# Kernel tuning notes

Hardware: AMD Instinct MI355X
Metric: run time of the kernel (lower is better)

Reference implementation:

```python
import jax, jax.numpy as jnp
import numpy as np

N_ATOMS = 100000
K_NBR = 64
N_STRUCT = 32
HID = 128


def _energy(x, W1, w2, mask, batch_idx):
    # x: [N, K, 3] neighbor displacement vectors; surrogate per-edge energy MLP
    h = jnp.tanh(jnp.einsum('nkc,cd->nkd', x, W1))          # [N, K, HID]
    e = jnp.einsum('nkd,d->nk', h, w2)                       # [N, K]
    e = jnp.where(mask, 0.0, e)                              # zero padded neighbors
    per_atom = e.sum(axis=1)                                 # [N]
    return jax.ops.segment_sum(per_atom, batch_idx, num_segments=N_STRUCT)  # [S]


def setup_inputs() -> dict:
    key = jax.random.key(0)
    k = jax.random.split(key, 7)
    x = jax.random.normal(k[0], (N_ATOMS, K_NBR, 3), dtype=jnp.float32)
    neighbors_index = jax.random.randint(k[1], (K_NBR, N_ATOMS), 0, N_ATOMS)
    neighbors_pos = jax.random.randint(k[2], (N_ATOMS, K_NBR), 0, K_NBR)
    mask = jax.random.randint(k[3], (N_ATOMS, K_NBR), 0, 2).astype(bool)
    batch_idx = jax.random.randint(k[4], (N_ATOMS,), 0, N_STRUCT)
    W1 = jax.random.normal(k[5], (3, HID), dtype=jnp.float32) * 0.1
    w2 = jax.random.normal(k[6], (HID,), dtype=jnp.float32) * 0.1
    return {"x": x, "neighbors_index": neighbors_index, "neighbors_pos": neighbors_pos,
            "mask": mask, "batch_idx": batch_idx, "W1": W1, "w2": w2}


def reference(x, neighbors_index, neighbors_pos, mask, batch_idx, W1, w2):
    # predictions: per-structure scalar energies
    preds = _energy(x, W1, w2, mask, batch_idx)
    # grads = d(sum of predictions)/dx  (grad_outputs = ones_like(predictions))
    grads = jax.grad(lambda xx: _energy(xx, W1, w2, mask, batch_idx).sum())(x)  # [N, K, 3]
    nbr = neighbors_index.T                                   # [N, K]
    # irregular gather of reverse-edge gradients (uses UNMASKED grads, as in torch code)
    grads_messaged = grads[nbr, neighbors_pos]                # [N, K, 3]
    m = mask[..., None]
    first = jnp.where(m, 0.0, grads).sum(axis=1)              # [N, 3]
    second = jnp.where(m, 0.0, grads_messaged).sum(axis=1)    # [N, 3]
    forces = first - second
    return preds, forces
```

## Files before the change

### kernel.cpp

```cpp
#include <hip/hip_runtime.h>
#include <hip/hip_bf16.h>

#define N_ATOMS 100000
#define K_NBR   64
#define N_STRUCT 32
#define HID     128
#define N_EDGE  (N_ATOMS * K_NBR)
#define ATOMS_PB 32
#define EDGES_PB (ATOMS_PB * K_NBR)
#define NBLK_EL (N_ATOMS / ATOMS_PB)
#define NBLK_A  ((N_ATOMS + 63) / 64)

typedef unsigned int uint;
typedef unsigned long long ull;
typedef _Float16 h2 __attribute__((ext_vector_type(2)));
typedef __fp16  p2 __attribute__((ext_vector_type(2)));

#if __has_builtin(__builtin_amdgcn_exp2f)
#define EXP2(v) __builtin_amdgcn_exp2f(v)
#else
#define EXP2(v) __expf((v) * 0.69314718056f)
#endif

#if __has_builtin(__builtin_amdgcn_fdot2)
#define FDOT2(a, b, c) __builtin_amdgcn_fdot2((a), (b), (c), false)
#else
__device__ __forceinline__ float FDOT2(h2 a, h2 b, float c) {
    return fmaf((float)a.y, (float)b.y, fmaf((float)a.x, (float)b.x, c));
}
#endif

union hcast { p2 p; h2 h; uint u; };

__device__ __forceinline__ h2 pkh(float a, float b) {
    hcast c; c.p = __builtin_amdgcn_cvt_pkrtz(a, b); return c.h;
}
__device__ __forceinline__ uint pku(float a, float b) {
    hcast c; c.p = __builtin_amdgcn_cvt_pkrtz(a, b); return c.u;
}
__device__ __forceinline__ h2 u2h(uint u) {
    hcast c; c.u = u; return c.h;
}

__device__ __forceinline__ uint bf_rne(float f) {
    uint u = __float_as_uint(f);
    return (u + 0x7fffu + ((u >> 16) & 1u)) >> 16;
}
__device__ __forceinline__ float ubf_lo(uint u) { return __uint_as_float(u << 16); }
__device__ __forceinline__ float ubf_hi(uint u) { return __uint_as_float(u & 0xffff0000u); }

__device__ __forceinline__ float red16(float x) {
    union { float f; int i; } a, b;
    a.f = x;
    b.i = __builtin_amdgcn_update_dpp(0, a.i, 0x118, 0xf, 0xf, false); a.f += b.f;
    b.i = __builtin_amdgcn_update_dpp(0, a.i, 0x114, 0xf, 0xf, false); a.f += b.f;
    b.i = __builtin_amdgcn_update_dpp(0, a.i, 0x112, 0xf, 0xf, false); a.f += b.f;
    b.i = __builtin_amdgcn_update_dpp(0, a.i, 0x111, 0xf, 0xf, false); a.f += b.f;
    return a.f;
}

__global__ void prep_kernel(const float* __restrict__ W1, const float* __restrict__ w2,
                            float4* __restrict__ pw4, uint4* __restrict__ gh4,
                            float* __restrict__ sumw2)
{
    __shared__ float sgx[HID], sgy[HID], sgz[HID];
    __shared__ float sw_[2];
    const float L2E2 = 2.885390082f;
    int d = threadIdx.x;
    float w0 = W1[d], w1 = W1[HID + d], wc = W1[2 * HID + d], wv = w2[d];
    pw4[d] = make_float4(L2E2 * w0, L2E2 * w1, L2E2 * wc, wv);
    sgx[d] = 4.f * wv * w0; sgy[d] = 4.f * wv * w1; sgz[d] = 4.f * wv * wc;
    float v = wv;
    for (int off = 32; off; off >>= 1) v += __shfl_down(v, off, 64);
    if ((d & 63) == 0) sw_[d >> 6] = v;
    __syncthreads();
    if (d == 0) sumw2[0] = sw_[0] + sw_[1];
    if (d < HID / 4) {
        int b = 4 * d;
        uint c0 = pku(sgx[b],     sgx[b + 1]);
        uint c1 = pku(sgx[b + 2], sgx[b + 3]);
        uint c2 = pku(sgy[b],     sgy[b + 1]);
        uint c3 = pku(sgy[b + 2], sgy[b + 3]);
        uint c4 = pku(sgz[b],     sgz[b + 1]);
        uint c5 = pku(sgz[b + 2], sgz[b + 3]);
        gh4[2 * d]     = make_uint4(c0, c1, c2, c3);
        gh4[2 * d + 1] = make_uint4(c4, c5, 0u, 0u);
    }
}

__global__ __launch_bounds__(256) void edge_local(
    const float* __restrict__ x, const int* __restrict__ mask,
    const int* __restrict__ batch,
    const float4* __restrict__ pw4, const uint4* __restrict__ gh4,
    const float* __restrict__ sumw2p,
    uint2* __restrict__ gr8, ull* __restrict__ bm, float* __restrict__ part)
{
    __shared__ unsigned short list[EDGES_PB];
    __shared__ int   lcnt;
    __shared__ float sp[N_STRUCT];
    __shared__ int   sbatch[ATOMS_PB];

    const int tid = threadIdx.x, lane = tid & 63;
    const int ebase = blockIdx.x * EDGES_PB;

    if (tid == 0) lcnt = 0;
    if (tid < N_STRUCT) sp[tid] = 0.f;
    if (tid < ATOMS_PB) sbatch[tid] = batch[blockIdx.x * ATOMS_PB + tid];
    __syncthreads();

    #pragma unroll
    for (int p = 0; p < EDGES_PB / 256; ++p) {
        int le = p * 256 + tid;
        int m = mask[ebase + le];
        unsigned long long bal = __ballot(m == 0);
        int wcnt = __popcll(bal);
        int pre  = __popcll(bal & ((1ull << lane) - 1ull));
        int wbase;
        if (lane == 0) {
            wbase = atomicAdd(&lcnt, wcnt);
            bm[(ebase + le) >> 6] = bal;
        }
        wbase = __shfl(wbase, 0, 64);
        if (m == 0) list[wbase + pre] = (unsigned short)le;
        else        gr8[ebase + le] = make_uint2(0u, 0u);
    }
    __syncthreads();

    const int L = lcnt;
    const float sumw2 = sumw2p[0];

    for (int i = tid; i < L; i += 256) {
        int le  = list[i];
        int eid = ebase + le;
        const float* xp = x + (size_t)eid * 3;
        float x0 = xp[0], x1 = xp[1], x2 = xp[2];
        float rsum = 0.f, g0 = 0.f, g1 = 0.f, g2 = 0.f;
        for (int d = 0; d < HID; d += 4) {
            float4 wa = pw4[d], wb = pw4[d + 1], wc = pw4[d + 2], wd = pw4[d + 3];
            uint4 GA = gh4[(d >> 1)];
            uint4 GB = gh4[(d >> 1) + 1];
            float ea = EXP2(fmaf(x0, wa.x, fmaf(x1, wa.y, x2 * wa.z)));
            float eb = EXP2(fmaf(x0, wb.x, fmaf(x1, wb.y, x2 * wb.z)));
            float ec = EXP2(fmaf(x0, wc.x, fmaf(x1, wc.y, x2 * wc.z)));
            float ed = EXP2(fmaf(x0, wd.x, fmaf(x1, wd.y, x2 * wd.z)));
            float aa = ea + 1.f, ab = eb + 1.f, ac = ec + 1.f, ad = ed + 1.f;
            float pab = aa * ab, pcd = ac * ad;
            float q   = __builtin_amdgcn_rcpf(pab * pcd);
            float qab = q * pcd, qcd = q * pab;
            float ra = qab * ab, rb = qab * aa, rc = qcd * ad, rd = qcd * ac;
            rsum = fmaf(wa.w, ra, rsum);
            rsum = fmaf(wb.w, rb, rsum);
            rsum = fmaf(wc.w, rc, rsum);
            rsum = fmaf(wd.w, rd, rsum);
            float sa = fmaf(-ra, ra, ra);
            float sb = fmaf(-rb, rb, rb);
            float sc = fmaf(-rc, rc, rc);
            float sd = fmaf(-rd, rd, rd);
            h2 sab = pkh(sa, sb);
            h2 scd = pkh(sc, sd);
            g0 = FDOT2(sab, u2h(GA.x), g0);
            g0 = FDOT2(scd, u2h(GA.y), g0);
            g1 = FDOT2(sab, u2h(GA.z), g1);
            g1 = FDOT2(scd, u2h(GA.w), g1);
            g2 = FDOT2(sab, u2h(GB.x), g2);
            g2 = FDOT2(scd, u2h(GB.y), g2);
        }
        float e = fmaf(-2.f, rsum, sumw2);
        uint lo = bf_rne(g0) | (bf_rne(g1) << 16);
        uint hi = bf_rne(g2);
        gr8[eid] = make_uint2(lo, hi);
        atomicAdd(&sp[sbatch[le >> 6]], e);
    }
    __syncthreads();
    if (tid < N_STRUCT) part[(size_t)tid * NBLK_EL + blockIdx.x] = sp[tid];
}

__global__ __launch_bounds__(256) void atom_fused(
    const uint2* __restrict__ gr8, const int* __restrict__ nidx,
    const int* __restrict__ pos,
    const ull* __restrict__ bm, const float* __restrict__ part,
    float* __restrict__ out)
{
    __shared__ int tile[64][65];
    __shared__ float sv[4];
    const int tid = threadIdx.x, lane = tid & 63, w = tid >> 6;
    const int n0 = blockIdx.x * 64;

    #pragma unroll
    for (int i = 0; i < 16; ++i) {
        int k = i * 4 + w, n = n0 + lane;
        tile[k][lane] = (n < N_ATOMS) ? nidx[k * N_ATOMS + n] : 0;
    }
    __syncthreads();

    const int grp = lane >> 4, kk = lane & 15;

    #pragma unroll
    for (int itp = 0; itp < 2; ++itp) {
        int  nl[2], n[2];
        bool v[2];
        ull  bmw[2];
        #pragma unroll
        for (int s = 0; s < 2; ++s) {
            nl[s]  = w * 16 + (itp * 2 + s) * 4 + grp;
            n[s]   = n0 + nl[s];
            v[s]   = (n[s] < N_ATOMS);
            bmw[s] = v[s] ? bm[n[s]] : 0ull;
        }

        uint2 A[2][4];
        #pragma unroll
        for (int s = 0; s < 2; ++s)
            #pragma unroll
            for (int ks = 0; ks < 4; ++ks) {
                int ei = n[s] * 64 + ks * 16 + kk;
                A[s][ks] = v[s] ? gr8[ei] : make_uint2(0u, 0u);
            }

        int  g[2][4];
        bool src[2][4];
        #pragma unroll
        for (int s = 0; s < 2; ++s)
            #pragma unroll
            for (int ks = 0; ks < 4; ++ks) {
                int k  = ks * 16 + kk;
                int ei = n[s] * 64 + k;
                src[s][ks] = (bmw[s] >> k) & 1ull;
                int p = src[s][ks] ? pos[ei] : 0;
                g[s][ks] = tile[k][nl[s]] * 64 + p;
            }

        ull fw[2][4];
        #pragma unroll
        for (int s = 0; s < 2; ++s)
            #pragma unroll
            for (int ks = 0; ks < 4; ++ks)
                fw[s][ks] = src[s][ks] ? bm[g[s][ks] >> 6] : 0ull;

        uint2 B[2][4];
        #pragma unroll
        for (int s = 0; s < 2; ++s)
            #pragma unroll
            for (int ks = 0; ks < 4; ++ks)
                B[s][ks] = ((fw[s][ks] >> (g[s][ks] & 63)) & 1ull)
                         ? gr8[g[s][ks]] : make_uint2(0u, 0u);

        #pragma unroll
        for (int s = 0; s < 2; ++s) {
            float f0 = 0.f, f1 = 0.f, f2 = 0.f;
            #pragma unroll
            for (int ks = 0; ks < 4; ++ks) {
                f0 += ubf_lo(A[s][ks].x) - ubf_lo(B[s][ks].x);
                f1 += ubf_hi(A[s][ks].x) - ubf_hi(B[s][ks].x);
                f2 += ubf_lo(A[s][ks].y) - ubf_lo(B[s][ks].y);
            }
            f0 = red16(f0); f1 = red16(f1); f2 = red16(f2);
            if (kk == 15 && v[s]) {
                float* fo = out + N_STRUCT + (size_t)n[s] * 3;
                fo[0] = f0; fo[1] = f1; fo[2] = f2;
            }
        }
    }

    if (blockIdx.x < N_STRUCT) {
        int s = blockIdx.x;
        float v = 0.f;
        for (int i = tid; i < NBLK_EL; i += 256) v += part[(size_t)s * NBLK_EL + i];
        for (int off = 32; off; off >>= 1) v += __shfl_down(v, off, 64);
        if (lane == 0) sv[w] = v;
        __syncthreads();
        if (tid == 0) out[s] = sv[0] + sv[1] + sv[2] + sv[3];
    }
}

extern "C" void kernel_launch(void* const* d_in, const int* in_sizes, int n_in,
                              void* d_out, int out_size, void* d_ws, size_t ws_size,
                              hipStream_t stream)
{
    const float* x    = (const float*)d_in[0];
    const int*   nidx = (const int*)d_in[1];
    const int*   npos = (const int*)d_in[2];
    const int*   mask = (const int*)d_in[3];
    const int*   bidx = (const int*)d_in[4];
    const float* W1   = (const float*)d_in[5];
    const float* w2   = (const float*)d_in[6];
    float* out = (float*)d_out;

    char* ws = (char*)d_ws;
    uint2* gr8  = (uint2*)ws;
    ull*   bm   = (ull*)(ws + (size_t)N_EDGE * 8);
    float* part = (float*)(ws + (size_t)N_EDGE * 8 + (size_t)(N_EDGE / 64) * 8);
    char*  tail = ws + (size_t)N_EDGE * 8 + (size_t)(N_EDGE / 64) * 8
                     + (size_t)N_STRUCT * NBLK_EL * sizeof(float);
    float4* pw4   = (float4*)tail;
    uint4*  gh4   = (uint4*)(tail + HID * 16);
    float*  sumw2 = (float*)(tail + 2 * HID * 16);

    hipLaunchKernelGGL(prep_kernel, dim3(1), dim3(128), 0, stream,
                       W1, w2, pw4, gh4, sumw2);
    hipLaunchKernelGGL(edge_local, dim3(NBLK_EL), dim3(256), 0, stream,
                       x, mask, bidx, pw4, gh4, sumw2, gr8, bm, part);
    hipLaunchKernelGGL(atom_fused, dim3(NBLK_A), dim3(256), 0, stream,
                       gr8, nidx, npos, bm, part, out);
}
```

Baseline: 344.4 us.

## Use packed FP32 math in edge MLP and skip zero-writes for masked edges

The per-edge hidden loop is rewritten to use packed two-wide float FMA and multiply ops, with weights re-laid out into paired float4 arrays so each lane computes two hidden units per instruction. The zero-store of gradients for masked edges is removed. In exchange, the atom kernel now gates its forward-gradient load on the bitmask, so unwritten gradient slots are never read. This trims VALU issue in the compute-bound edge loop and cuts store traffic for about half the edges.

```diff
diff --git a/kernel.cpp b/kernel.cpp
--- a/kernel.cpp
+++ b/kernel.cpp
@@ -15,6 +15,7 @@
 typedef unsigned long long ull;
 typedef _Float16 h2 __attribute__((ext_vector_type(2)));
 typedef __fp16  p2 __attribute__((ext_vector_type(2)));
+typedef float   f2 __attribute__((ext_vector_type(2)));
 
 #if __has_builtin(__builtin_amdgcn_exp2f)
 #define EXP2(v) __builtin_amdgcn_exp2f(v)
@@ -29,6 +30,9 @@
     return fmaf((float)a.y, (float)b.y, fmaf((float)a.x, (float)b.x, c));
 }
 #endif
+
+#define PKFMA(a, b, c) __builtin_elementwise_fma((a), (b), (c))
+#define SWAP2(v) __builtin_shufflevector((v), (v), 1, 0)
 
 union hcast { p2 p; h2 h; uint u; };
 
@@ -60,21 +64,27 @@
 }
 
 __global__ void prep_kernel(const float* __restrict__ W1, const float* __restrict__ w2,
-                            float4* __restrict__ pw4, uint4* __restrict__ gh4,
-                            float* __restrict__ sumw2)
+                            float4* __restrict__ pwa4, float4* __restrict__ pwb4,
+                            uint4* __restrict__ gh4, float* __restrict__ sumw2)
 {
+    __shared__ float spx[HID], spy[HID], spz[HID], spv[HID];
     __shared__ float sgx[HID], sgy[HID], sgz[HID];
     __shared__ float sw_[2];
     const float L2E2 = 2.885390082f;
     int d = threadIdx.x;
     float w0 = W1[d], w1 = W1[HID + d], wc = W1[2 * HID + d], wv = w2[d];
-    pw4[d] = make_float4(L2E2 * w0, L2E2 * w1, L2E2 * wc, wv);
+    spx[d] = L2E2 * w0; spy[d] = L2E2 * w1; spz[d] = L2E2 * wc; spv[d] = wv;
     sgx[d] = 4.f * wv * w0; sgy[d] = 4.f * wv * w1; sgz[d] = 4.f * wv * wc;
     float v = wv;
     for (int off = 32; off; off >>= 1) v += __shfl_down(v, off, 64);
     if ((d & 63) == 0) sw_[d >> 6] = v;
     __syncthreads();
     if (d == 0) sumw2[0] = sw_[0] + sw_[1];
+    if (d < HID / 2) {
+        int b = 2 * d;
+        pwa4[d] = make_float4(spx[b], spx[b + 1], spy[b], spy[b + 1]);
+        pwb4[d] = make_float4(spz[b], spz[b + 1], spv[b], spv[b + 1]);
+    }
     if (d < HID / 4) {
         int b = 4 * d;
         uint c0 = pku(sgx[b],     sgx[b + 1]);
@@ -91,7 +101,8 @@
 __global__ __launch_bounds__(256) void edge_local(
     const float* __restrict__ x, const int* __restrict__ mask,
     const int* __restrict__ batch,
-    const float4* __restrict__ pw4, const uint4* __restrict__ gh4,
+    const float4* __restrict__ pwa4, const float4* __restrict__ pwb4,
+    const uint4* __restrict__ gh4,
     const float* __restrict__ sumw2p,
     uint2* __restrict__ gr8, ull* __restrict__ bm, float* __restrict__ part)
 {
@@ -122,7 +133,6 @@
         }
         wbase = __shfl(wbase, 0, 64);
         if (m == 0) list[wbase + pre] = (unsigned short)le;
-        else        gr8[ebase + le] = make_uint2(0u, 0u);
     }
     __syncthreads();
 
@@ -134,30 +144,35 @@
         int eid = ebase + le;
         const float* xp = x + (size_t)eid * 3;
         float x0 = xp[0], x1 = xp[1], x2 = xp[2];
-        float rsum = 0.f, g0 = 0.f, g1 = 0.f, g2 = 0.f;
-        for (int d = 0; d < HID; d += 4) {
-            float4 wa = pw4[d], wb = pw4[d + 1], wc = pw4[d + 2], wd = pw4[d + 3];
-            uint4 GA = gh4[(d >> 1)];
-            uint4 GB = gh4[(d >> 1) + 1];
-            float ea = EXP2(fmaf(x0, wa.x, fmaf(x1, wa.y, x2 * wa.z)));
-            float eb = EXP2(fmaf(x0, wb.x, fmaf(x1, wb.y, x2 * wb.z)));
-            float ec = EXP2(fmaf(x0, wc.x, fmaf(x1, wc.y, x2 * wc.z)));
-            float ed = EXP2(fmaf(x0, wd.x, fmaf(x1, wd.y, x2 * wd.z)));
-            float aa = ea + 1.f, ab = eb + 1.f, ac = ec + 1.f, ad = ed + 1.f;
-            float pab = aa * ab, pcd = ac * ad;
+        const f2 x0v = {x0, x0}, x1v = {x1, x1}, x2v = {x2, x2};
+        const f2 onev = {1.f, 1.f};
+        f2 rs = {0.f, 0.f};
+        float g0 = 0.f, g1 = 0.f, g2 = 0.f;
+        for (int j = 0; j < HID / 2; j += 2) {
+            float4 Aa = pwa4[j],     Ab = pwb4[j];
+            float4 Ba = pwa4[j + 1], Bb = pwb4[j + 1];
+            uint4 GA = gh4[j];
+            uint4 GB = gh4[j + 1];
+            f2 wx01 = {Aa.x, Aa.y}, wy01 = {Aa.z, Aa.w};
+            f2 wz01 = {Ab.x, Ab.y}, wv01 = {Ab.z, Ab.w};
+            f2 wx23 = {Ba.x, Ba.y}, wy23 = {Ba.z, Ba.w};
+            f2 wz23 = {Bb.x, Bb.y}, wv23 = {Bb.z, Bb.w};
+            f2 p01 = PKFMA(x0v, wx01, PKFMA(x1v, wy01, x2v * wz01));
+            f2 p23 = PKFMA(x0v, wx23, PKFMA(x1v, wy23, x2v * wz23));
+            f2 e01 = {EXP2(p01.x), EXP2(p01.y)};
+            f2 e23 = {EXP2(p23.x), EXP2(p23.y)};
+            f2 a01 = e01 + onev, a23 = e23 + onev;
+            float pab = a01.x * a01.y, pcd = a23.x * a23.y;
             float q   = __builtin_amdgcn_rcpf(pab * pcd);
             float qab = q * pcd, qcd = q * pab;
-            float ra = qab * ab, rb = qab * aa, rc = qcd * ad, rd = qcd * ac;
-            rsum = fmaf(wa.w, ra, rsum);
-            rsum = fmaf(wb.w, rb, rsum);
-            rsum = fmaf(wc.w, rc, rsum);
-            rsum = fmaf(wd.w, rd, rsum);
-            float sa = fmaf(-ra, ra, ra);
-            float sb = fmaf(-rb, rb, rb);
-            float sc = fmaf(-rc, rc, rc);
-            float sd = fmaf(-rd, rd, rd);
-            h2 sab = pkh(sa, sb);
-            h2 scd = pkh(sc, sd);
+            f2 r01 = (f2){qab, qab} * SWAP2(a01);
+            f2 r23 = (f2){qcd, qcd} * SWAP2(a23);
+            rs = PKFMA(wv01, r01, rs);
+            rs = PKFMA(wv23, r23, rs);
+            f2 s01 = PKFMA(-r01, r01, r01);
+            f2 s23 = PKFMA(-r23, r23, r23);
+            h2 sab = pkh(s01.x, s01.y);
+            h2 scd = pkh(s23.x, s23.y);
             g0 = FDOT2(sab, u2h(GA.x), g0);
             g0 = FDOT2(scd, u2h(GA.y), g0);
             g1 = FDOT2(sab, u2h(GA.z), g1);
@@ -165,7 +180,7 @@
             g2 = FDOT2(sab, u2h(GB.x), g2);
             g2 = FDOT2(scd, u2h(GB.y), g2);
         }
-        float e = fmaf(-2.f, rsum, sumw2);
+        float e = fmaf(-2.f, rs.x + rs.y, sumw2);
         uint lo = bf_rne(g0) | (bf_rne(g1) << 16);
         uint hi = bf_rne(g2);
         gr8[eid] = make_uint2(lo, hi);
@@ -209,23 +224,24 @@
         }
 
         uint2 A[2][4];
+        bool  src[2][4];
         #pragma unroll
         for (int s = 0; s < 2; ++s)
             #pragma unroll
             for (int ks = 0; ks < 4; ++ks) {
-                int ei = n[s] * 64 + ks * 16 + kk;
-                A[s][ks] = v[s] ? gr8[ei] : make_uint2(0u, 0u);
+                int k  = ks * 16 + kk;
+                src[s][ks] = (bmw[s] >> k) & 1ull;
+                int ei = n[s] * 64 + k;
+                A[s][ks] = src[s][ks] ? gr8[ei] : make_uint2(0u, 0u);
             }
 
-        int  g[2][4];
-        bool src[2][4];
+        int g[2][4];
         #pragma unroll
         for (int s = 0; s < 2; ++s)
             #pragma unroll
             for (int ks = 0; ks < 4; ++ks) {
                 int k  = ks * 16 + kk;
                 int ei = n[s] * 64 + k;
-                src[s][ks] = (bmw[s] >> k) & 1ull;
                 int p = src[s][ks] ? pos[ei] : 0;
                 g[s][ks] = tile[k][nl[s]] * 64 + p;
             }
@@ -247,17 +263,17 @@
 
         #pragma unroll
         for (int s = 0; s < 2; ++s) {
-            float f0 = 0.f, f1 = 0.f, f2 = 0.f;
+            float f0 = 0.f, f1 = 0.f, f2_ = 0.f;
             #pragma unroll
             for (int ks = 0; ks < 4; ++ks) {
-                f0 += ubf_lo(A[s][ks].x) - ubf_lo(B[s][ks].x);
-                f1 += ubf_hi(A[s][ks].x) - ubf_hi(B[s][ks].x);
-                f2 += ubf_lo(A[s][ks].y) - ubf_lo(B[s][ks].y);
+                f0  += ubf_lo(A[s][ks].x) - ubf_lo(B[s][ks].x);
+                f1  += ubf_hi(A[s][ks].x) - ubf_hi(B[s][ks].x);
+                f2_ += ubf_lo(A[s][ks].y) - ubf_lo(B[s][ks].y);
             }
-            f0 = red16(f0); f1 = red16(f1); f2 = red16(f2);
+            f0 = red16(f0); f1 = red16(f1); f2_ = red16(f2_);
             if (kk == 15 && v[s]) {
                 float* fo = out + N_STRUCT + (size_t)n[s] * 3;
-                fo[0] = f0; fo[1] = f1; fo[2] = f2;
+                fo[0] = f0; fo[1] = f1; fo[2] = f2_;
             }
         }
     }
@@ -292,14 +308,15 @@
     float* part = (float*)(ws + (size_t)N_EDGE * 8 + (size_t)(N_EDGE / 64) * 8);
     char*  tail = ws + (size_t)N_EDGE * 8 + (size_t)(N_EDGE / 64) * 8
                      + (size_t)N_STRUCT * NBLK_EL * sizeof(float);
-    float4* pw4   = (float4*)tail;
-    uint4*  gh4   = (uint4*)(tail + HID * 16);
-    float*  sumw2 = (float*)(tail + 2 * HID * 16);
+    float4* pwa4  = (float4*)tail;
+    float4* pwb4  = (float4*)(tail + (HID / 2) * 16);
+    uint4*  gh4   = (uint4*)(tail + 2 * (HID / 2) * 16);
+    float*  sumw2 = (float*)(tail + 3 * (HID / 2) * 16);
 
     hipLaunchKernelGGL(prep_kernel, dim3(1), dim3(128), 0, stream,
-                       W1, w2, pw4, gh4, sumw2);
+                       W1, w2, pwa4, pwb4, gh4, sumw2);
     hipLaunchKernelGGL(edge_local, dim3(NBLK_EL), dim3(256), 0, stream,
-                       x, mask, bidx, pw4, gh4, sumw2, gr8, bm, part);
+                       x, mask, bidx, pwa4, pwb4, gh4, sumw2, gr8, bm, part);
     hipLaunchKernelGGL(atom_fused, dim3(NBLK_A), dim3(256), 0, stream,
                        gr8, nidx, npos, bm, part, out);
 }
```

Result: faster. 332.3 us (-3.5%).
